# Kernel tuning notes

Measured on AMD Instinct MI355X. Metric: run time of the kernel, lower is better.

## Reference

```python
import jax, jax.numpy as jnp
import numpy as np

N_NODES = 100000
N_EDGES = 1000000

def _gcn_conv(x, W, b, src, dst, n_nodes):
    # PyG GCNConv: linear first, then symmetric-normalized aggregation with self loops
    x = x @ W  # [N, F_out]
    loop = jnp.arange(n_nodes, dtype=src.dtype)
    src2 = jnp.concatenate([src, loop])
    dst2 = jnp.concatenate([dst, loop])
    deg = jax.ops.segment_sum(jnp.ones(src2.shape[0], x.dtype), dst2, num_segments=n_nodes)
    dinv = jnp.where(deg > 0, jax.lax.rsqrt(deg), 0.0)
    norm = dinv[src2] * dinv[dst2]  # [E+N]
    msgs = x[src2] * norm[:, None]  # gather + scale
    out = jax.ops.segment_sum(msgs, dst2, num_segments=n_nodes)  # scatter-add
    return out + b

def _pair_norm_si(x):
    # mode 'PN-SI', scale=1
    x = x - x.mean(axis=0)
    row_norm = jnp.sqrt(1e-6 + jnp.sum(x * x, axis=1, keepdims=True))
    return x / row_norm

def setup_inputs() -> dict:
    key = jax.random.key(0)
    k1, k2, k3, k4 = jax.random.split(key, 4)
    in_c, hid_c, out_c = 256, 64, 40
    x = jax.random.normal(k1, (N_NODES, in_c), dtype=jnp.float32)
    edge_index = jax.random.randint(k2, (2, N_EDGES), 0, N_NODES, dtype=jnp.int64)
    W1 = jax.random.normal(k3, (in_c, hid_c), dtype=jnp.float32) / np.sqrt(in_c)
    b1 = jnp.zeros((hid_c,), jnp.float32)
    W2 = jax.random.normal(k4, (hid_c, out_c), dtype=jnp.float32) / np.sqrt(hid_c)
    b2 = jnp.zeros((out_c,), jnp.float32)
    return {"x": x, "edge_index": edge_index, "W1": W1, "b1": b1, "W2": W2, "b2": b2}

def reference(x, edge_index, W1, b1, W2, b2):
    src, dst = edge_index[0], edge_index[1]
    n = x.shape[0]
    h = jax.nn.relu(_gcn_conv(x, W1, b1, src, dst, n))
    h = _gcn_conv(h, W2, b2, src, dst, n)
    h = _pair_norm_si(h)
    return jax.nn.log_softmax(h, axis=1)
```

## Files before the change

kernel.cpp:

```cpp
#include <hip/hip_runtime.h>
#include <hip/hip_fp16.h>
#include <math.h>

#define F_IN  256
#define F_HID 64
#define F_OUT 40
#define HS2_LD 64

typedef _Float16 h8 __attribute__((ext_vector_type(8)));
typedef _Float16 h4 __attribute__((ext_vector_type(4)));
typedef float f4 __attribute__((ext_vector_type(4)));

__global__ void k_degw(const int* __restrict__ dst, unsigned* __restrict__ degc, int E,
                       const float* __restrict__ W1, const float* __restrict__ W2,
                       __half* __restrict__ Wt, __half* __restrict__ W2t) {
    int i = blockIdx.x * 256 + threadIdx.x;
    if (i < E) {
        atomicAdd(&degc[dst[i]], 1u);
        return;
    }
    int j = i - E;
    if (j < 16384) {
        int k = j >> 6, n = j & 63;
        Wt[n * 256 + k] = __float2half(W1[j]);
    } else if (j < 20480) {
        int jj = j - 16384;
        int n = jj >> 6, k = jj & 63;
        W2t[n * 64 + k] = __float2half((n < F_OUT) ? W2[k * F_OUT + n] : 0.f);
    }
}

__global__ __launch_bounds__(256) void k_scan(const unsigned* __restrict__ degc,
                                              unsigned* __restrict__ aggf,
                                              unsigned* __restrict__ ticket,
                                              unsigned* __restrict__ rowptr,
                                              float* __restrict__ dinv,
                                              unsigned* __restrict__ cursor,
                                              float* __restrict__ colsum, int N) {
    __shared__ unsigned s[256];
    __shared__ unsigned sTick, sPfx, sTot;
    int tid = threadIdx.x;
    if (tid == 0) sTick = atomicAdd(ticket, 1u);
    if (blockIdx.x == 0 && tid < 64) colsum[tid] = 0.f;
    __syncthreads();
    unsigned b = sTick;
    int i = (int)b * 256 + tid;
    unsigned d = (i < N) ? degc[i] : 0u;
    unsigned v = (i < N) ? ((d + 8u) & ~7u) : 0u;
    s[tid] = v;
    __syncthreads();
    for (int off = 1; off < 256; off <<= 1) {
        unsigned t = (tid >= off) ? s[tid - off] : 0u;
        __syncthreads();
        s[tid] += t;
        __syncthreads();
    }
    unsigned incl = s[tid];
    if (tid == 255) {
        sTot = s[255];
        atomicExch(&aggf[b], s[255] | 0x40000000u);
    }
    __syncthreads();
    if (tid == 0) {
        unsigned run = 0;
        int pr = (int)b - 1;
        while (pr >= 0) {
            unsigned t;
            do { t = atomicAdd(&aggf[pr], 0u); } while ((t >> 30) == 0u);
            run += t & 0x3FFFFFFFu;
            if ((t >> 30) == 3u) break;
            --pr;
        }
        sPfx = run;
        atomicExch(&aggf[b], (run + sTot) | 0xC0000000u);
    }
    __syncthreads();
    unsigned pfx = sPfx;
    if (i < N) {
        rowptr[i] = pfx + incl - v;
        dinv[i] = rsqrtf((float)d + 1.0f);
        cursor[i] = 0u;
        if (i == N - 1) rowptr[N] = pfx + incl;
    }
    if (i == 0) dinv[N] = 1.0f;
}

__global__ __launch_bounds__(256) void k_fillpad(const int* __restrict__ src, const int* __restrict__ dst,
                          const unsigned* __restrict__ degc,
                          const unsigned* __restrict__ rowptr, unsigned* __restrict__ cursor,
                          unsigned* __restrict__ colp, int E, int N) {
    int r  = blockIdx.x & 7;
    int sb = blockIdx.x >> 3;
    int S  = gridDim.x >> 3;
    int lo = (int)(((long long)N * r) >> 3);
    int hi = (int)(((long long)N * (r + 1)) >> 3);
    int tid = threadIdx.x;
    int stride = S * 256;
    for (int t = sb * 256 + tid; t < E; t += stride) {
        int d = dst[t];
        if (d >= lo && d < hi) {
            unsigned p = atomicAdd(&cursor[d], 1u);
            colp[rowptr[d] + p] = (unsigned)src[t];
        }
    }
    int npad = (hi - lo) * 8;
    for (int z = sb * 256 + tid; z < npad; z += stride) {
        int i = lo + (z >> 3), j = z & 7;
        unsigned d = degc[i];
        unsigned slot = d + (unsigned)j;
        if (slot < ((d + 8u) & ~7u))
            colp[rowptr[i] + slot] = (j == 0) ? (unsigned)i : (unsigned)N;
    }
}

__global__ __launch_bounds__(256) void k_mm1(const float* __restrict__ x,
                                             const __half* __restrict__ Wth,
                                             const float* __restrict__ dinv,
                                             __half* __restrict__ hs1o, int N) {
    const _Float16* Wt = (const _Float16*)Wth;
    _Float16* hs1 = (_Float16*)hs1o;
    int tid = threadIdx.x;
    int lane = tid & 63;
    int wv = tid >> 6;
    int m15 = lane & 15;
    int q = lane >> 4;
    int node0 = blockIdx.x * 64 + wv * 16;
    int arow = node0 + m15;
    bool ok = (arow < N);
    const float* xr = x + (size_t)arow * F_IN + q * 8;

    f4 acc[4];
    #pragma unroll
    for (int nt = 0; nt < 4; ++nt) acc[nt] = (f4){0.f, 0.f, 0.f, 0.f};

    #pragma unroll
    for (int kt = 0; kt < 8; ++kt) {
        float4 v0, v1;
        if (ok) {
            v0 = *(const float4*)(xr + kt * 32);
            v1 = *(const float4*)(xr + kt * 32 + 4);
        } else {
            v0 = make_float4(0.f, 0.f, 0.f, 0.f);
            v1 = v0;
        }
        h8 a = { (_Float16)v0.x, (_Float16)v0.y, (_Float16)v0.z, (_Float16)v0.w,
                 (_Float16)v1.x, (_Float16)v1.y, (_Float16)v1.z, (_Float16)v1.w };
        #pragma unroll
        for (int nt = 0; nt < 4; ++nt) {
            h8 b = *(const h8*)(Wt + (nt * 16 + m15) * 256 + kt * 32 + q * 8);
            acc[nt] = __builtin_amdgcn_mfma_f32_16x16x32_f16(a, b, acc[nt], 0, 0, 0);
        }
    }

    #pragma unroll
    for (int nt = 0; nt < 4; ++nt) {
        #pragma unroll
        for (int rr = 0; rr < 4; ++rr) {
            int node = node0 + q * 4 + rr;
            if (node <= N) {
                float din = (node < N) ? dinv[node] : 1.0f;
                hs1[(size_t)node * F_HID + nt * 16 + m15] = (_Float16)(acc[nt][rr] * din);
            }
        }
    }
}

__global__ __launch_bounds__(256) void k_agg1(const unsigned* __restrict__ rowptr,
                                              const unsigned* __restrict__ colp,
                                              const float* __restrict__ dinv,
                                              const __half* __restrict__ hs1o,
                                              const float* __restrict__ bias1,
                                              __half* __restrict__ agg1o, int N) {
    const _Float16* hp = (const _Float16*)hs1o;
    _Float16* agg1h = (_Float16*)agg1o;
    int lane = threadIdx.x & 63;
    int w = blockIdx.x * 4 + (threadIdx.x >> 6);
    int na = 2 * w, nb = 2 * w + 1;
    if (na >= N) return;
    int g = lane >> 3, c = lane & 7;

    float accA[8], accB[8];
    #pragma unroll
    for (int j = 0; j < 8; ++j) { accA[j] = 0.f; accB[j] = 0.f; }

    unsigned aE = rowptr[na], aEnd = rowptr[na + 1];
    bool hasB = (nb < N);
    unsigned bE = 0, bEnd = 0;
    if (hasB) { bE = rowptr[nb]; bEnd = rowptr[nb + 1]; }

    while (aE < aEnd && bE < bEnd) {
        unsigned sA = colp[aE + g];
        unsigned sB = colp[bE + g];
        h8 va = *(const h8*)(hp + (size_t)sA * F_HID + c * 8);
        h8 vb = *(const h8*)(hp + (size_t)sB * F_HID + c * 8);
        #pragma unroll
        for (int j = 0; j < 8; ++j) { accA[j] += (float)va[j]; accB[j] += (float)vb[j]; }
        aE += 8; bE += 8;
    }
    while (aE < aEnd) {
        unsigned sA = colp[aE + g];
        h8 va = *(const h8*)(hp + (size_t)sA * F_HID + c * 8);
        #pragma unroll
        for (int j = 0; j < 8; ++j) accA[j] += (float)va[j];
        aE += 8;
    }
    while (bE < bEnd) {
        unsigned sB = colp[bE + g];
        h8 vb = *(const h8*)(hp + (size_t)sB * F_HID + c * 8);
        #pragma unroll
        for (int j = 0; j < 8; ++j) accB[j] += (float)vb[j];
        bE += 8;
    }

    #pragma unroll
    for (int off = 8; off <= 32; off <<= 1) {
        #pragma unroll
        for (int j = 0; j < 8; ++j) {
            accA[j] += __shfl_xor(accA[j], off, 64);
            accB[j] += __shfl_xor(accB[j], off, 64);
        }
    }

    if (g == 0) {
        float bv[8];
        *(float4*)&bv[0] = *(const float4*)(bias1 + c * 8);
        *(float4*)&bv[4] = *(const float4*)(bias1 + c * 8 + 4);
        float dinA = dinv[na];
        h8 ho;
        #pragma unroll
        for (int j = 0; j < 8; ++j) ho[j] = (_Float16)fmaxf(accA[j] * dinA + bv[j], 0.f);
        *(h8*)(agg1h + (size_t)na * F_HID + c * 8) = ho;
        if (hasB) {
            float dinB = dinv[nb];
            #pragma unroll
            for (int j = 0; j < 8; ++j) ho[j] = (_Float16)fmaxf(accB[j] * dinB + bv[j], 0.f);
            *(h8*)(agg1h + (size_t)nb * F_HID + c * 8) = ho;
        }
    }
}

#define AS 72
__global__ __launch_bounds__(256) void k_mm2(const __half* __restrict__ agg1o,
                                             const __half* __restrict__ W2th,
                                             const float* __restrict__ dinv,
                                             __half* __restrict__ hs2o, int N) {
    __shared__ _Float16 sA[64 * AS];
    const _Float16* agg1h = (const _Float16*)agg1o;
    const _Float16* W2t = (const _Float16*)W2th;
    _Float16* hs2 = (_Float16*)hs2o;
    int tid = threadIdx.x;
    int lane = tid & 63;
    int wv = tid >> 6;
    int m15 = lane & 15;
    int q = lane >> 4;
    int nbase = blockIdx.x * 64;

    h8 bf[2];
    #pragma unroll
    for (int kt = 0; kt < 2; ++kt)
        bf[kt] = *(const h8*)(W2t + (wv * 16 + m15) * 64 + kt * 32 + q * 8);

    #pragma unroll
    for (int p = 0; p < 2; ++p) {
        int idx = p * 256 + tid;
        int row = idx >> 3;
        int c8  = idx & 7;
        int node = nbase + row;
        h8 v;
        if (node < N) v = *(const h8*)(agg1h + (size_t)node * F_HID + c8 * 8);
        else          v = (h8){0, 0, 0, 0, 0, 0, 0, 0};
        *(h8*)&sA[row * AS + c8 * 8] = v;
    }
    __syncthreads();

    f4 acc[4];
    #pragma unroll
    for (int mt = 0; mt < 4; ++mt) acc[mt] = (f4){0.f, 0.f, 0.f, 0.f};
    #pragma unroll
    for (int kt = 0; kt < 2; ++kt) {
        #pragma unroll
        for (int mt = 0; mt < 4; ++mt) {
            h8 a = *(const h8*)&sA[(mt * 16 + m15) * AS + kt * 32 + q * 8];
            acc[mt] = __builtin_amdgcn_mfma_f32_16x16x32_f16(a, bf[kt], acc[mt], 0, 0, 0);
        }
    }

    #pragma unroll
    for (int mt = 0; mt < 4; ++mt) {
        #pragma unroll
        for (int r = 0; r < 4; ++r) {
            int node = nbase + mt * 16 + q * 4 + r;
            if (node <= N) {
                float din = (node < N) ? dinv[node] : 1.0f;
                hs2[(size_t)node * HS2_LD + wv * 16 + m15] = (_Float16)(acc[mt][r] * din);
            }
        }
    }
}

__global__ __launch_bounds__(256) void k_agg2(const unsigned* __restrict__ rowptr,
                                              const unsigned* __restrict__ colp,
                                              const float* __restrict__ dinv,
                                              const __half* __restrict__ hs2o,
                                              float* __restrict__ out,
                                              float* __restrict__ colsum, int N) {
    __shared__ float part[4][8][8];
    const _Float16* hp = (const _Float16*)hs2o;
    int lane = threadIdx.x & 63;
    int wv = threadIdx.x >> 6;
    int g = lane >> 3, c = lane & 7;
    int nwaves = gridDim.x * 4;
    float csum[8];
    #pragma unroll
    for (int j = 0; j < 8; ++j) csum[j] = 0.f;

    for (int w = blockIdx.x * 4 + wv; 2 * w < N; w += nwaves) {
        int na = 2 * w, nb = 2 * w + 1;
        float accA[8], accB[8];
        #pragma unroll
        for (int j = 0; j < 8; ++j) { accA[j] = 0.f; accB[j] = 0.f; }

        unsigned aE = rowptr[na], aEnd = rowptr[na + 1];
        bool hasB = (nb < N);
        unsigned bE = 0, bEnd = 0;
        if (hasB) { bE = rowptr[nb]; bEnd = rowptr[nb + 1]; }

        while (aE < aEnd && bE < bEnd) {
            unsigned sA = colp[aE + g];
            unsigned sB = colp[bE + g];
            h8 va = *(const h8*)(hp + (size_t)sA * HS2_LD + c * 8);
            h8 vb = *(const h8*)(hp + (size_t)sB * HS2_LD + c * 8);
            #pragma unroll
            for (int j = 0; j < 8; ++j) { accA[j] += (float)va[j]; accB[j] += (float)vb[j]; }
            aE += 8; bE += 8;
        }
        while (aE < aEnd) {
            unsigned sA = colp[aE + g];
            h8 va = *(const h8*)(hp + (size_t)sA * HS2_LD + c * 8);
            #pragma unroll
            for (int j = 0; j < 8; ++j) accA[j] += (float)va[j];
            aE += 8;
        }
        while (bE < bEnd) {
            unsigned sB = colp[bE + g];
            h8 vb = *(const h8*)(hp + (size_t)sB * HS2_LD + c * 8);
            #pragma unroll
            for (int j = 0; j < 8; ++j) accB[j] += (float)vb[j];
            bE += 8;
        }

        #pragma unroll
        for (int off = 8; off <= 32; off <<= 1) {
            #pragma unroll
            for (int j = 0; j < 8; ++j) {
                accA[j] += __shfl_xor(accA[j], off, 64);
                accB[j] += __shfl_xor(accB[j], off, 64);
            }
        }

        if (g == 0) {
            float dinA = dinv[na];
            #pragma unroll
            for (int j = 0; j < 8; ++j) { accA[j] *= dinA; csum[j] += accA[j]; }
            if (c < 5) {
                *(float4*)(out + (size_t)na * F_OUT + c * 8) =
                    make_float4(accA[0], accA[1], accA[2], accA[3]);
                *(float4*)(out + (size_t)na * F_OUT + c * 8 + 4) =
                    make_float4(accA[4], accA[5], accA[6], accA[7]);
            }
            if (hasB) {
                float dinB = dinv[nb];
                #pragma unroll
                for (int j = 0; j < 8; ++j) { accB[j] *= dinB; csum[j] += accB[j]; }
                if (c < 5) {
                    *(float4*)(out + (size_t)nb * F_OUT + c * 8) =
                        make_float4(accB[0], accB[1], accB[2], accB[3]);
                    *(float4*)(out + (size_t)nb * F_OUT + c * 8 + 4) =
                        make_float4(accB[4], accB[5], accB[6], accB[7]);
                }
            }
        }
    }

    if (g == 0) {
        #pragma unroll
        for (int j = 0; j < 8; ++j) part[wv][c][j] = csum[j];
    }
    __syncthreads();
    int tid = threadIdx.x;
    if (tid < F_OUT) {
        int cc = tid >> 3, jj = tid & 7;
        float s = part[0][cc][jj] + part[1][cc][jj] + part[2][cc][jj] + part[3][cc][jj];
        atomicAdd(&colsum[tid], s);
    }
}

__global__ __launch_bounds__(128) void k_final(float* __restrict__ out,
                                               const float* __restrict__ colsum, int N) {
    __shared__ float sMean[F_OUT];
    if (threadIdx.x < F_OUT) sMean[threadIdx.x] = colsum[threadIdx.x] * (1.0f / (float)N);
    __syncthreads();
    int n = blockIdx.x * blockDim.x + threadIdx.x;
    if (n >= N) return;
    float* row = out + (size_t)n * F_OUT;
    float v[F_OUT];
    float ss = 0.f;
    #pragma unroll
    for (int f = 0; f < F_OUT; ++f) {
        float t = row[f] - sMean[f];
        v[f] = t;
        ss += t * t;
    }
    float scale = 1.0f / sqrtf(ss + 1e-6f);
    float m = -1e30f;
    #pragma unroll
    for (int f = 0; f < F_OUT; ++f) {
        float y = v[f] * scale;
        v[f] = y;
        m = fmaxf(m, y);
    }
    float sum = 0.f;
    #pragma unroll
    for (int f = 0; f < F_OUT; ++f) sum += expf(v[f] - m);
    float lse = logf(sum);
    #pragma unroll
    for (int f = 0; f < F_OUT; ++f) row[f] = v[f] - m - lse;
}

extern "C" void kernel_launch(void* const* d_in, const int* in_sizes, int n_in,
                              void* d_out, int out_size, void* d_ws, size_t ws_size,
                              hipStream_t stream) {
    const float* x  = (const float*)d_in[0];
    const int*   ei = (const int*)d_in[1];
    const float* W1 = (const float*)d_in[2];
    const float* b1 = (const float*)d_in[3];
    const float* W2 = (const float*)d_in[4];
    float* out = (float*)d_out;

    int N = in_sizes[0] / F_IN;
    int E = in_sizes[1] / 2;
    const int* src = ei;
    const int* dst = ei + E;

    char* p = (char*)d_ws;
    auto alloc = [&](size_t bytes) { char* r = p; p += (bytes + 127) & ~(size_t)127; return r; };
    unsigned* degc   = (unsigned*)alloc((size_t)N * 4);
    unsigned* aggf   = (unsigned*)alloc(512 * 4);
    unsigned* ticket = (unsigned*)alloc(4);
    char* zend = p;
    unsigned* cursor = (unsigned*)alloc((size_t)N * 4);
    float*    colsum = (float*)   alloc(64 * 4);
    unsigned* rowptr = (unsigned*)alloc((size_t)(N + 1) * 4);
    unsigned* colp   = (unsigned*)alloc((size_t)(E + 8 * N + 8) * 4);
    float*    dinv   = (float*)   alloc((size_t)(N + 1) * 4);
    __half*   agg1h  = (__half*)  alloc((size_t)64 * (N + 1) * 2);
    __half*   hs1    = (__half*)  alloc((size_t)64 * (N + 1) * 2);
    __half*   hs2    = (__half*)  alloc((size_t)64 * (N + 1) * 2);
    __half*   Wt     = (__half*)  alloc((size_t)16384 * 2);
    __half*   W2t    = (__half*)  alloc((size_t)4096 * 2);

    hipMemsetAsync(d_ws, 0, (size_t)(zend - (char*)d_ws), stream);

    int nA = (N + 255) / 256;
    k_degw<<<(E + 20480 + 255) / 256, 256, 0, stream>>>(dst, degc, E, W1, W2, Wt, W2t);
    k_scan<<<nA, 256, 0, stream>>>(degc, aggf, ticket, rowptr, dinv, cursor, colsum, N);
    k_fillpad<<<2048, 256, 0, stream>>>(src, dst, degc, rowptr, cursor, colp, E, N);
    k_mm1<<<(N + 63) / 64, 256, 0, stream>>>(x, Wt, dinv, hs1, N);
    int waves1 = (N + 1) / 2;
    k_agg1<<<(waves1 + 3) / 4, 256, 0, stream>>>(rowptr, colp, dinv, hs1, b1, agg1h, N);
    k_mm2<<<(N + 64) / 64, 256, 0, stream>>>(agg1h, W2t, dinv, hs2, N);
    k_agg2<<<2048, 256, 0, stream>>>(rowptr, colp, dinv, hs2, out, colsum, N);
    k_final<<<(N + 127) / 128, 128, 0, stream>>>(out, colsum, N);
}
```

Measured before the change: 393.9 us.

## Process four nodes per wave in aggregation and parallelize scan lookback

The two aggregation kernels now have each wavefront gather four destination nodes at once instead of two. The four edge streams are interleaved in a single loop so more independent gathers are in flight per wave. Separately, the decoupled-lookback prefix scan now has a whole wavefront poll 64 predecessor flags in parallel and reduce them with shuffles, replacing the single thread that walked back one block at a time. The cost is more registers per thread, which may lower occupancy, plus some divergence when the four nodes have different degrees.

```diff
diff --git a/kernel.cpp b/kernel.cpp
--- a/kernel.cpp
+++ b/kernel.cpp
@@ -61,18 +61,36 @@
         atomicExch(&aggf[b], s[255] | 0x40000000u);
     }
     __syncthreads();
-    if (tid == 0) {
+    if (tid < 64) {
+        int lane = tid;
         unsigned run = 0;
-        int pr = (int)b - 1;
-        while (pr >= 0) {
-            unsigned t;
-            do { t = atomicAdd(&aggf[pr], 0u); } while ((t >> 30) == 0u);
-            run += t & 0x3FFFFFFFu;
-            if ((t >> 30) == 3u) break;
-            --pr;
-        }
-        sPfx = run;
-        atomicExch(&aggf[b], (run + sTot) | 0xC0000000u);
+        int base = (int)b - 1;
+        while (base >= 0) {
+            int idx = base - lane;
+            unsigned t = 0;
+            if (idx >= 0) {
+                do { t = atomicAdd(&aggf[idx], 0u); } while ((t >> 30) == 0u);
+            }
+            unsigned long long pmask = __ballot(idx >= 0 && (t >> 30) == 3u);
+            if (pmask) {
+                int L = __ffsll((unsigned long long)pmask) - 1;
+                unsigned contrib = (lane <= L) ? (t & 0x3FFFFFFFu) : 0u;
+                #pragma unroll
+                for (int off = 32; off >= 1; off >>= 1) contrib += __shfl_xor(contrib, off, 64);
+                run += contrib;
+                break;
+            } else {
+                unsigned contrib = (idx >= 0) ? (t & 0x3FFFFFFFu) : 0u;
+                #pragma unroll
+                for (int off = 32; off >= 1; off >>= 1) contrib += __shfl_xor(contrib, off, 64);
+                run += contrib;
+                base -= 64;
+            }
+        }
+        if (lane == 0) {
+            sPfx = run;
+            atomicExch(&aggf[b], (run + sTot) | 0xC0000000u);
+        }
     }
     __syncthreads();
     unsigned pfx = sPfx;
@@ -175,66 +193,58 @@
     _Float16* agg1h = (_Float16*)agg1o;
     int lane = threadIdx.x & 63;
     int w = blockIdx.x * 4 + (threadIdx.x >> 6);
-    int na = 2 * w, nb = 2 * w + 1;
-    if (na >= N) return;
+    int n0 = 4 * w;
+    if (n0 >= N) return;
     int g = lane >> 3, c = lane & 7;
 
-    float accA[8], accB[8];
-    #pragma unroll
-    for (int j = 0; j < 8; ++j) { accA[j] = 0.f; accB[j] = 0.f; }
-
-    unsigned aE = rowptr[na], aEnd = rowptr[na + 1];
-    bool hasB = (nb < N);
-    unsigned bE = 0, bEnd = 0;
-    if (hasB) { bE = rowptr[nb]; bEnd = rowptr[nb + 1]; }
-
-    while (aE < aEnd && bE < bEnd) {
-        unsigned sA = colp[aE + g];
-        unsigned sB = colp[bE + g];
-        h8 va = *(const h8*)(hp + (size_t)sA * F_HID + c * 8);
-        h8 vb = *(const h8*)(hp + (size_t)sB * F_HID + c * 8);
-        #pragma unroll
-        for (int j = 0; j < 8; ++j) { accA[j] += (float)va[j]; accB[j] += (float)vb[j]; }
-        aE += 8; bE += 8;
-    }
-    while (aE < aEnd) {
-        unsigned sA = colp[aE + g];
-        h8 va = *(const h8*)(hp + (size_t)sA * F_HID + c * 8);
-        #pragma unroll
-        for (int j = 0; j < 8; ++j) accA[j] += (float)va[j];
-        aE += 8;
-    }
-    while (bE < bEnd) {
-        unsigned sB = colp[bE + g];
-        h8 vb = *(const h8*)(hp + (size_t)sB * F_HID + c * 8);
-        #pragma unroll
-        for (int j = 0; j < 8; ++j) accB[j] += (float)vb[j];
-        bE += 8;
-    }
-
-    #pragma unroll
-    for (int off = 8; off <= 32; off <<= 1) {
-        #pragma unroll
-        for (int j = 0; j < 8; ++j) {
-            accA[j] += __shfl_xor(accA[j], off, 64);
-            accB[j] += __shfl_xor(accB[j], off, 64);
-        }
-    }
+    float acc[4][8];
+    #pragma unroll
+    for (int s = 0; s < 4; ++s)
+        #pragma unroll
+        for (int j = 0; j < 8; ++j) acc[s][j] = 0.f;
+
+    unsigned e[4], en[4];
+    #pragma unroll
+    for (int s = 0; s < 4; ++s) {
+        int nd = n0 + s;
+        if (nd < N) { e[s] = rowptr[nd]; en[s] = rowptr[nd + 1]; }
+        else        { e[s] = 0; en[s] = 0; }
+    }
+
+    while (e[0] < en[0] || e[1] < en[1] || e[2] < en[2] || e[3] < en[3]) {
+        #pragma unroll
+        for (int s = 0; s < 4; ++s) {
+            if (e[s] < en[s]) {
+                unsigned sA = colp[e[s] + g];
+                h8 v = *(const h8*)(hp + (size_t)sA * F_HID + c * 8);
+                #pragma unroll
+                for (int j = 0; j < 8; ++j) acc[s][j] += (float)v[j];
+                e[s] += 8;
+            }
+        }
+    }
+
+    #pragma unroll
+    for (int off = 8; off <= 32; off <<= 1)
+        #pragma unroll
+        for (int s = 0; s < 4; ++s)
+            #pragma unroll
+            for (int j = 0; j < 8; ++j) acc[s][j] += __shfl_xor(acc[s][j], off, 64);
 
     if (g == 0) {
         float bv[8];
         *(float4*)&bv[0] = *(const float4*)(bias1 + c * 8);
         *(float4*)&bv[4] = *(const float4*)(bias1 + c * 8 + 4);
-        float dinA = dinv[na];
-        h8 ho;
-        #pragma unroll
-        for (int j = 0; j < 8; ++j) ho[j] = (_Float16)fmaxf(accA[j] * dinA + bv[j], 0.f);
-        *(h8*)(agg1h + (size_t)na * F_HID + c * 8) = ho;
-        if (hasB) {
-            float dinB = dinv[nb];
-            #pragma unroll
-            for (int j = 0; j < 8; ++j) ho[j] = (_Float16)fmaxf(accB[j] * dinB + bv[j], 0.f);
-            *(h8*)(agg1h + (size_t)nb * F_HID + c * 8) = ho;
+        #pragma unroll
+        for (int s = 0; s < 4; ++s) {
+            int nd = n0 + s;
+            if (nd < N) {
+                float din = dinv[nd];
+                h8 ho;
+                #pragma unroll
+                for (int j = 0; j < 8; ++j) ho[j] = (_Float16)fmaxf(acc[s][j] * din + bv[j], 0.f);
+                *(h8*)(agg1h + (size_t)nd * F_HID + c * 8) = ho;
+            }
         }
     }
 }
@@ -314,69 +324,56 @@
     #pragma unroll
     for (int j = 0; j < 8; ++j) csum[j] = 0.f;
 
-    for (int w = blockIdx.x * 4 + wv; 2 * w < N; w += nwaves) {
-        int na = 2 * w, nb = 2 * w + 1;
-        float accA[8], accB[8];
-        #pragma unroll
-        for (int j = 0; j < 8; ++j) { accA[j] = 0.f; accB[j] = 0.f; }
-
-        unsigned aE = rowptr[na], aEnd = rowptr[na + 1];
-        bool hasB = (nb < N);
-        unsigned bE = 0, bEnd = 0;
-        if (hasB) { bE = rowptr[nb]; bEnd = rowptr[nb + 1]; }
-
-        while (aE < aEnd && bE < bEnd) {
-            unsigned sA = colp[aE + g];
-            unsigned sB = colp[bE + g];
-            h8 va = *(const h8*)(hp + (size_t)sA * HS2_LD + c * 8);
-            h8 vb = *(const h8*)(hp + (size_t)sB * HS2_LD + c * 8);
+    for (int w = blockIdx.x * 4 + wv; 4 * w < N; w += nwaves) {
+        int n0 = 4 * w;
+        float acc[4][8];
+        #pragma unroll
+        for (int s = 0; s < 4; ++s)
             #pragma unroll
-            for (int j = 0; j < 8; ++j) { accA[j] += (float)va[j]; accB[j] += (float)vb[j]; }
-            aE += 8; bE += 8;
-        }
-        while (aE < aEnd) {
-            unsigned sA = colp[aE + g];
-            h8 va = *(const h8*)(hp + (size_t)sA * HS2_LD + c * 8);
+            for (int j = 0; j < 8; ++j) acc[s][j] = 0.f;
+
+        unsigned e[4], en[4];
+        #pragma unroll
+        for (int s = 0; s < 4; ++s) {
+            int nd = n0 + s;
+            if (nd < N) { e[s] = rowptr[nd]; en[s] = rowptr[nd + 1]; }
+            else        { e[s] = 0; en[s] = 0; }
+        }
+
+        while (e[0] < en[0] || e[1] < en[1] || e[2] < en[2] || e[3] < en[3]) {
             #pragma unroll
-            for (int j = 0; j < 8; ++j) accA[j] += (float)va[j];
-            aE += 8;
-        }
-        while (bE < bEnd) {
-            unsigned sB = colp[bE + g];
-            h8 vb = *(const h8*)(hp + (size_t)sB * HS2_LD + c * 8);
+            for (int s = 0; s < 4; ++s) {
+                if (e[s] < en[s]) {
+                    unsigned sA = colp[e[s] + g];
+                    h8 v = *(const h8*)(hp + (size_t)sA * HS2_LD + c * 8);
+                    #pragma unroll
+                    for (int j = 0; j < 8; ++j) acc[s][j] += (float)v[j];
+                    e[s] += 8;
+                }
+            }
+        }
+
+        #pragma unroll
+        for (int off = 8; off <= 32; off <<= 1)
             #pragma unroll
-            for (int j = 0; j < 8; ++j) accB[j] += (float)vb[j];
-            bE += 8;
-        }
-
-        #pragma unroll
-        for (int off = 8; off <= 32; off <<= 1) {
+            for (int s = 0; s < 4; ++s)
+                #pragma unroll
+                for (int j = 0; j < 8; ++j) acc[s][j] += __shfl_xor(acc[s][j], off, 64);
+
+        if (g == 0) {
             #pragma unroll
-            for (int j = 0; j < 8; ++j) {
-                accA[j] += __shfl_xor(accA[j], off, 64);
-                accB[j] += __shfl_xor(accB[j], off, 64);
-            }
-        }
-
-        if (g == 0) {
-            float dinA = dinv[na];
-            #pragma unroll
-            for (int j = 0; j < 8; ++j) { accA[j] *= dinA; csum[j] += accA[j]; }
-            if (c < 5) {
-                *(float4*)(out + (size_t)na * F_OUT + c * 8) =
-                    make_float4(accA[0], accA[1], accA[2], accA[3]);
-                *(float4*)(out + (size_t)na * F_OUT + c * 8 + 4) =
-                    make_float4(accA[4], accA[5], accA[6], accA[7]);
-            }
-            if (hasB) {
-                float dinB = dinv[nb];
-                #pragma unroll
-                for (int j = 0; j < 8; ++j) { accB[j] *= dinB; csum[j] += accB[j]; }
-                if (c < 5) {
-                    *(float4*)(out + (size_t)nb * F_OUT + c * 8) =
-                        make_float4(accB[0], accB[1], accB[2], accB[3]);
-                    *(float4*)(out + (size_t)nb * F_OUT + c * 8 + 4) =
-                        make_float4(accB[4], accB[5], accB[6], accB[7]);
+            for (int s = 0; s < 4; ++s) {
+                int nd = n0 + s;
+                if (nd < N) {
+                    float din = dinv[nd];
+                    #pragma unroll
+                    for (int j = 0; j < 8; ++j) { acc[s][j] *= din; csum[j] += acc[s][j]; }
+                    if (c < 5) {
+                        *(float4*)(out + (size_t)nd * F_OUT + c * 8) =
+                            make_float4(acc[s][0], acc[s][1], acc[s][2], acc[s][3]);
+                        *(float4*)(out + (size_t)nd * F_OUT + c * 8 + 4) =
+                            make_float4(acc[s][4], acc[s][5], acc[s][6], acc[s][7]);
+                    }
                 }
             }
         }
@@ -466,8 +463,8 @@
     k_scan<<<nA, 256, 0, stream>>>(degc, aggf, ticket, rowptr, dinv, cursor, colsum, N);
     k_fillpad<<<2048, 256, 0, stream>>>(src, dst, degc, rowptr, cursor, colp, E, N);
     k_mm1<<<(N + 63) / 64, 256, 0, stream>>>(x, Wt, dinv, hs1, N);
-    int waves1 = (N + 1) / 2;
-    k_agg1<<<(waves1 + 3) / 4, 256, 0, stream>>>(rowptr, colp, dinv, hs1, b1, agg1h, N);
+    int nodes4 = (N + 3) / 4;
+    k_agg1<<<(nodes4 + 3) / 4, 256, 0, stream>>>(rowptr, colp, dinv, hs1, b1, agg1h, N);
     k_mm2<<<(N + 64) / 64, 256, 0, stream>>>(agg1h, W2t, dinv, hs2, N);
     k_agg2<<<2048, 256, 0, stream>>>(rowptr, colp, dinv, hs2, out, colsum, N);
     k_final<<<(N + 127) / 128, 128, 0, stream>>>(out, colsum, N);
```

Result: slower. 427.1 us (+8.4%).
